# Kernel optimization log

Hardware: AMD Instinct MI355X
Metric: run time of the kernel (lower is better)

## Reference

```python
import jax, jax.numpy as jnp
import numpy as np

# GE2E batch structure: N_SPK speakers, M_UTT utterances each (grouped contiguously),
# first half enrollment (-> centroid), second half test.
N_SPK, M_UTT, D = 1024, 32, 512
M_ENR = M_UTT // 2
EPS = 1e-8  # F.cosine_similarity default eps (clamps norms)


def setup_inputs() -> dict:
    key = jax.random.key(0)
    emb = jax.random.normal(key, (N_SPK * M_UTT, D), dtype=jnp.float32)
    labels = jnp.repeat(jnp.arange(N_SPK, dtype=jnp.int64), M_UTT)
    alpha = jnp.asarray(10.0, dtype=jnp.float32)
    beta = jnp.asarray(-5.0, dtype=jnp.float32)
    return {"embeddings": emb, "labels": labels, "alpha": alpha, "beta": beta}


def reference(embeddings, labels, alpha, beta):
    # labels are contiguously grouped: label i occupies rows [i*M_UTT, (i+1)*M_UTT)
    emb = embeddings.reshape(N_SPK, M_UTT, D)
    enroll = emb[:, :M_ENR]          # [N, M_enr, D]
    test = emb[:, M_ENR:]            # [N, M_tst, D]
    centroid = enroll.mean(axis=1)   # [N, D]

    cent_n = centroid / jnp.maximum(
        jnp.linalg.norm(centroid, axis=-1, keepdims=True), EPS)
    test_n = test / jnp.maximum(
        jnp.linalg.norm(test, axis=-1, keepdims=True), EPS)

    # S[i, j, t] = alpha * cos(centroid_i, test_{j,t}) + beta
    S = alpha * jnp.einsum('id,jtd->ijt', cent_n, test_n) + beta
    E = jnp.exp(S)                                   # [N, N, M_tst]

    idx = jnp.arange(N_SPK)
    pos_sum = E[idx, idx].sum(axis=-1)               # diag: own test vs own centroid
    neg_sum = E.sum(axis=(1, 2)) - pos_sum           # all other speakers' test utts

    loss = (jnp.log(neg_sum) - jnp.log(pos_sum)).mean()
    return loss
```

## Files before the change

### kernel.cpp

```cpp
#include <hip/hip_runtime.h>
#include <math.h>

#define N_SPK 1024
#define M_UTT 32
#define M_ENR 16
#define M_TEST 16
#define D 512
#define N_TEST_ROWS (N_SPK * M_TEST)


typedef __attribute__((ext_vector_type(4))) float f32x4;
typedef __attribute__((ext_vector_type(8))) short short8;
typedef __attribute__((ext_vector_type(8))) unsigned short ushort8;

typedef const __attribute__((address_space(1))) void g_void;
typedef __attribute__((address_space(3))) void lds_void;

__device__ __forceinline__ unsigned short f2bf(float f) {
    unsigned int u = __float_as_uint(f);
    u += 0x7FFF + ((u >> 16) & 1);
    return (unsigned short)(u >> 16);
}

__global__ __launch_bounds__(256) void prep_kernel(const float* __restrict__ emb,
                                                   unsigned short* __restrict__ cent,
                                                   unsigned short* __restrict__ test,
                                                   float* __restrict__ g_row,
                                                   float* __restrict__ g_pos) {
    const int b = blockIdx.x;
    const int tid = threadIdx.x;
    const int lane = tid & 63;
    const int wid = tid >> 6;

    if (b < 4) {
        g_row[b * 256 + tid] = 0.f;
        g_pos[b * 256 + tid] = 0.f;
    }

    if (b < N_SPK) {
        const float* base = emb + (size_t)b * M_UTT * D;
        float a0 = 0.f, a1 = 0.f;
#pragma unroll
        for (int u = 0; u < M_ENR; ++u) {
            a0 += base[u * D + tid];
            a1 += base[u * D + tid + 256];
        }
        a0 *= (1.f / 16.f);
        a1 *= (1.f / 16.f);
        float ss = a0 * a0 + a1 * a1;
#pragma unroll
        for (int m = 1; m < 64; m <<= 1) ss += __shfl_xor(ss, m, 64);
        __shared__ float wss[4];
        if (lane == 0) wss[wid] = ss;
        __syncthreads();
        const float tot = wss[0] + wss[1] + wss[2] + wss[3];
        const float inv = 1.f / fmaxf(sqrtf(tot), 1e-8f);
        cent[b * D + tid] = f2bf(a0 * inv);
        cent[b * D + tid + 256] = f2bf(a1 * inv);
    } else {
        const int r = (b - N_SPK) * 4 + wid;
        const int s = r >> 4, t = r & 15;
        const float* row = emb + ((size_t)s * M_UTT + M_ENR + t) * D;
        const f32x4* rv = (const f32x4*)row;
        const f32x4 v0 = rv[lane * 2];
        const f32x4 v1 = rv[lane * 2 + 1];
        float ss = v0[0]*v0[0] + v0[1]*v0[1] + v0[2]*v0[2] + v0[3]*v0[3]
                 + v1[0]*v1[0] + v1[1]*v1[1] + v1[2]*v1[2] + v1[3]*v1[3];
#pragma unroll
        for (int m = 1; m < 64; m <<= 1) ss += __shfl_xor(ss, m, 64);
        const float inv = 1.f / fmaxf(sqrtf(ss), 1e-8f);
        ushort8 o;
        o[0] = f2bf(v0[0] * inv); o[1] = f2bf(v0[1] * inv);
        o[2] = f2bf(v0[2] * inv); o[3] = f2bf(v0[3] * inv);
        o[4] = f2bf(v1[0] * inv); o[5] = f2bf(v1[1] * inv);
        o[6] = f2bf(v1[2] * inv); o[7] = f2bf(v1[3] * inv);
        *(ushort8*)&test[(size_t)r * D + lane * 8] = o;
    }
}

__global__ __launch_bounds__(512, 2) void gemm_kernel(const unsigned short* __restrict__ A,
                                                      const unsigned short* __restrict__ B,
                                                      const float* __restrict__ alpha_p,
                                                      const float* __restrict__ beta_p,
                                                      float* __restrict__ g_row,
                                                      float* __restrict__ g_pos) {
    __shared__ __align__(16) unsigned short As[128 * 512];
    __shared__ float rowsum[128];
    __shared__ float possum[128];

    const int tid = threadIdx.x;
    const int lane = tid & 63;
    const int w = tid >> 6;

    const int raw = blockIdx.x;
    const int wg = (raw & 7) * 32 + (raw >> 3);
    const int bi = wg & 7;
    const int bj = wg >> 3;
    const int row0 = bi * 128, col0 = bj * 512;
    const bool has_diag = ((bj >> 2) == bi);

#pragma unroll
    for (int it = 0; it < 16; ++it) {
        const int r = it * 8 + w;
        const int src = (row0 + r) * D + ((lane * 8) ^ ((r & 7) << 3));
        __builtin_amdgcn_global_load_lds((g_void*)&A[src],
                                         (lds_void*)&As[r * D],
                                         16, 0, 0);
    }
    if (tid < 128) { rowsum[tid] = 0.f; possum[tid] = 0.f; }

    const float alpha = *alpha_p;
    const float beta = *beta_p;

    const int bcol = col0 + w * 64;
    const unsigned short* bp[4];
#pragma unroll
    for (int ni = 0; ni < 4; ++ni)
        bp[ni] = &B[(size_t)(bcol + ni * 16 + (lane & 15)) * D + (lane >> 4) * 8];

    const int hs = ((lane >> 4) * 8) ^ ((lane & 7) << 3);
    const int arow_base = (lane & 15) * D;

    f32x4 acc[8][4] = {};
    short8 bf0[4], bf1[4];

#define LOADB(dst, kk)                                             \
    {                                                              \
        const int kp_ = (kk);                                      \
        _Pragma("unroll") for (int ni = 0; ni < 4; ++ni)           \
            dst[ni] = *(const short8*)(bp[ni] + kp_);              \
    }

#define STEP(bfr, kk)                                                          \
    {                                                                          \
        const int ofs_ = (kk) ^ hs;                                            \
        _Pragma("unroll") for (int mi = 0; mi < 8; ++mi) {                     \
            const short8 af_ = *(const short8*)&As[mi * 16 * D + arow_base + ofs_]; \
            _Pragma("unroll") for (int ni = 0; ni < 4; ++ni)                   \
                acc[mi][ni] = __builtin_amdgcn_mfma_f32_16x16x32_bf16(         \
                    af_, bfr[ni], acc[mi][ni], 0, 0, 0);                       \
        }                                                                      \
    }

    LOADB(bf0, 0);
    __syncthreads();

    for (int ko = 0; ko < D; ko += 64) {
        LOADB(bf1, ko + 32);
        STEP(bf0, ko);
        LOADB(bf0, (ko + 64) & (D - 1));
        STEP(bf1, ko + 32);
    }

#pragma unroll
    for (int mi = 0; mi < 8; ++mi) {
#pragma unroll
        for (int r = 0; r < 4; ++r) {
            const int lrow = mi * 16 + ((lane >> 4) << 2) + r;
            const int grow = row0 + lrow;
            float tot = 0.f, pos = 0.f;
#pragma unroll
            for (int ni = 0; ni < 4; ++ni) {
                const int gcol = bcol + ni * 16 + (lane & 15);
                const float e = __expf(fmaf(alpha, acc[mi][ni][r], beta));
                tot += e;
                if (has_diag) pos += ((gcol >> 4) == grow) ? e : 0.f;
            }
#pragma unroll
            for (int m = 1; m < 16; m <<= 1) tot += __shfl_xor(tot, m, 64);
            if (has_diag) {
#pragma unroll
                for (int m = 1; m < 16; m <<= 1) pos += __shfl_xor(pos, m, 64);
            }
            if ((lane & 15) == 0) {
                atomicAdd(&rowsum[lrow], tot);
                if (has_diag) atomicAdd(&possum[lrow], pos);
            }
        }
    }
    __syncthreads();
    if (tid < 128) {
        atomicAdd(&g_row[row0 + tid], rowsum[tid]);
        if (has_diag) atomicAdd(&g_pos[row0 + tid], possum[tid]);
    }
#undef LOADB
#undef STEP
}

__global__ __launch_bounds__(1024) void finalize_kernel(const float* __restrict__ g_row,
                                                        const float* __restrict__ g_pos,
                                                        float* __restrict__ out) {
    __shared__ float red[1024];
    const int i = threadIdx.x;
    const float pos = g_pos[i];
    const float neg = g_row[i] - pos;
    red[i] = logf(fmaxf(neg, 1e-30f)) - logf(fmaxf(pos, 1e-30f));
    __syncthreads();
    for (int s = 512; s > 0; s >>= 1) {
        if (i < s) red[i] += red[i + s];
        __syncthreads();
    }
    if (i == 0) out[0] = red[0] * (1.f / 1024.f);
}

extern "C" void kernel_launch(void* const* d_in, const int* in_sizes, int n_in,
                              void* d_out, int out_size, void* d_ws, size_t ws_size,
                              hipStream_t stream) {
    const float* emb = (const float*)d_in[0];
    const float* alpha_p = (const float*)d_in[2];
    const float* beta_p = (const float*)d_in[3];

    unsigned short* cent = (unsigned short*)d_ws;
    unsigned short* test = cent + (size_t)N_SPK * D;
    float* g_row = (float*)(test + (size_t)N_TEST_ROWS * D);
    float* g_pos = g_row + N_SPK;

    prep_kernel<<<N_SPK + N_TEST_ROWS / 4, 256, 0, stream>>>(emb, cent, test, g_row, g_pos);

    gemm_kernel<<<256, 512, 0, stream>>>(cent, test, alpha_p, beta_p, g_row, g_pos);

    finalize_kernel<<<1, 1024, 0, stream>>>(g_row, g_pos, (float*)d_out);
}
```

Measured before the change: 49.09 us.

## Switch similarity GEMM to FP8 scaled MFMA and fuse finalize via last-block reduction

Normalized centroids and test rows are now quantized to FP8 E4M3 instead of BF16, and the GEMM uses the 32x32x64 scaled f8f6f4 MFMA with test rows as the M operand and centroids staged in LDS. The tile mapping changes to 512 blocks, and the separate finalize kernel is removed: a global counter lets the last finishing block compute the log-loss. The aim is to halve operand bandwidth, double matrix throughput and save a kernel launch, at the cost of FP8 precision error inside exp(alpha*cos), which could shift the loss.

```diff
diff --git a/kernel.cpp b/kernel.cpp
--- a/kernel.cpp
+++ b/kernel.cpp
@@ -7,26 +7,43 @@
 #define M_TEST 16
 #define D 512
 #define N_TEST_ROWS (N_SPK * M_TEST)
+#define NBLK_GEMM 512
 
 
 typedef __attribute__((ext_vector_type(4))) float f32x4;
-typedef __attribute__((ext_vector_type(8))) short short8;
-typedef __attribute__((ext_vector_type(8))) unsigned short ushort8;
+typedef __attribute__((ext_vector_type(4))) int i32x4;
+typedef __attribute__((ext_vector_type(8))) int i32x8;
+typedef __attribute__((ext_vector_type(16))) float f32x16;
 
 typedef const __attribute__((address_space(1))) void g_void;
 typedef __attribute__((address_space(3))) void lds_void;
 
-__device__ __forceinline__ unsigned short f2bf(float f) {
+__device__ __forceinline__ unsigned int f2e4m3(float f) {
     unsigned int u = __float_as_uint(f);
-    u += 0x7FFF + ((u >> 16) & 1);
-    return (unsigned short)(u >> 16);
+    const unsigned int s = (u >> 31) << 7;
+    float a = fabsf(f);
+    if (a >= 448.f) return s | 0x7E;
+    unsigned int ua = u & 0x7FFFFFFFu;
+    int e = (int)(ua >> 23) - 127;
+    if (e >= -6) {
+        ua += 0x7FFFF + ((ua >> 20) & 1);
+        e = (int)(ua >> 23) - 127;
+        if (e > 8) return s | 0x7E;
+        const unsigned int m = (ua >> 20) & 7;
+        return s | ((unsigned int)(e + 7) << 3) | m;
+    } else {
+        const int k = (int)rintf(a * 512.f);
+        if (k >= 8) return s | 0x08;
+        return s | (unsigned int)k;
+    }
 }
 
 __global__ __launch_bounds__(256) void prep_kernel(const float* __restrict__ emb,
-                                                   unsigned short* __restrict__ cent,
-                                                   unsigned short* __restrict__ test,
+                                                   unsigned char* __restrict__ cent8,
+                                                   unsigned char* __restrict__ test8,
                                                    float* __restrict__ g_row,
-                                                   float* __restrict__ g_pos) {
+                                                   float* __restrict__ g_pos,
+                                                   unsigned int* __restrict__ cnt) {
     const int b = blockIdx.x;
     const int tid = threadIdx.x;
     const int lane = tid & 63;
@@ -35,6 +52,7 @@
     if (b < 4) {
         g_row[b * 256 + tid] = 0.f;
         g_pos[b * 256 + tid] = 0.f;
+        if (b == 0 && tid == 0) *cnt = 0u;
     }
 
     if (b < N_SPK) {
@@ -55,8 +73,8 @@
         __syncthreads();
         const float tot = wss[0] + wss[1] + wss[2] + wss[3];
         const float inv = 1.f / fmaxf(sqrtf(tot), 1e-8f);
-        cent[b * D + tid] = f2bf(a0 * inv);
-        cent[b * D + tid + 256] = f2bf(a1 * inv);
+        cent8[b * D + tid] = (unsigned char)f2e4m3(a0 * inv);
+        cent8[b * D + tid + 256] = (unsigned char)f2e4m3(a1 * inv);
     } else {
         const int r = (b - N_SPK) * 4 + wid;
         const int s = r >> 4, t = r & 15;
@@ -69,138 +87,166 @@
 #pragma unroll
         for (int m = 1; m < 64; m <<= 1) ss += __shfl_xor(ss, m, 64);
         const float inv = 1.f / fmaxf(sqrtf(ss), 1e-8f);
-        ushort8 o;
-        o[0] = f2bf(v0[0] * inv); o[1] = f2bf(v0[1] * inv);
-        o[2] = f2bf(v0[2] * inv); o[3] = f2bf(v0[3] * inv);
-        o[4] = f2bf(v1[0] * inv); o[5] = f2bf(v1[1] * inv);
-        o[6] = f2bf(v1[2] * inv); o[7] = f2bf(v1[3] * inv);
-        *(ushort8*)&test[(size_t)r * D + lane * 8] = o;
-    }
-}
-
-__global__ __launch_bounds__(512, 2) void gemm_kernel(const unsigned short* __restrict__ A,
-                                                      const unsigned short* __restrict__ B,
-                                                      const float* __restrict__ alpha_p,
-                                                      const float* __restrict__ beta_p,
-                                                      float* __restrict__ g_row,
-                                                      float* __restrict__ g_pos) {
-    __shared__ __align__(16) unsigned short As[128 * 512];
-    __shared__ float rowsum[128];
-    __shared__ float possum[128];
+        unsigned long long ob = 0ull;
+        ob |= (unsigned long long)f2e4m3(v0[0] * inv);
+        ob |= (unsigned long long)f2e4m3(v0[1] * inv) << 8;
+        ob |= (unsigned long long)f2e4m3(v0[2] * inv) << 16;
+        ob |= (unsigned long long)f2e4m3(v0[3] * inv) << 24;
+        ob |= (unsigned long long)f2e4m3(v1[0] * inv) << 32;
+        ob |= (unsigned long long)f2e4m3(v1[1] * inv) << 40;
+        ob |= (unsigned long long)f2e4m3(v1[2] * inv) << 48;
+        ob |= (unsigned long long)f2e4m3(v1[3] * inv) << 56;
+        *(unsigned long long*)&test8[(size_t)r * D + lane * 8] = ob;
+    }
+}
+
+__global__ __launch_bounds__(512) void gemm_kernel(const unsigned char* __restrict__ A,
+                                                   const unsigned char* __restrict__ Bc,
+                                                   const float* __restrict__ alpha_p,
+                                                   const float* __restrict__ beta_p,
+                                                   float* __restrict__ g_row,
+                                                   float* __restrict__ g_pos,
+                                                   unsigned int* __restrict__ cnt,
+                                                   float* __restrict__ out) {
+    __shared__ __align__(16) unsigned char Bs[128 * 512];
+    __shared__ float tsum[128];
+    __shared__ float psum[128];
+    __shared__ unsigned int last_flag;
+    __shared__ float ws2[8];
 
     const int tid = threadIdx.x;
     const int lane = tid & 63;
     const int w = tid >> 6;
-
-    const int raw = blockIdx.x;
-    const int wg = (raw & 7) * 32 + (raw >> 3);
-    const int bi = wg & 7;
-    const int bj = wg >> 3;
-    const int row0 = bi * 128, col0 = bj * 512;
-    const bool has_diag = ((bj >> 2) == bi);
-
-#pragma unroll
-    for (int it = 0; it < 16; ++it) {
-        const int r = it * 8 + w;
-        const int src = (row0 + r) * D + ((lane * 8) ^ ((r & 7) << 3));
-        __builtin_amdgcn_global_load_lds((g_void*)&A[src],
-                                         (lds_void*)&As[r * D],
-                                         16, 0, 0);
-    }
-    if (tid < 128) { rowsum[tid] = 0.f; possum[tid] = 0.f; }
+    const int wr = w >> 1;
+    const int wc = w & 1;
+    const int hh = lane >> 5;
+    const int l31 = lane & 31;
+
+    const int bid = blockIdx.x;
+    const int idx = bid >> 3;
+    const int bm = (bid & 7) * 8 + (idx & 7);
+    const int bn = idx >> 3;
+    const bool has_diag = (bn == (bm >> 3));
+
+#pragma unroll
+    for (int it = 0; it < 8; ++it) {
+        const int q = it * 8 + w;
+        const int r_l = 2 * q + hh;
+        const int src_col = (l31 ^ (r_l & 31)) << 4;
+        __builtin_amdgcn_global_load_lds(
+            (g_void*)&Bc[(size_t)(bn * 128 + r_l) * D + src_col],
+            (lds_void*)&Bs[(2 * q) * 512],
+            16, 0, 0);
+    }
+    if (tid < 128) { tsum[tid] = 0.f; psum[tid] = 0.f; }
 
     const float alpha = *alpha_p;
     const float beta = *beta_p;
 
-    const int bcol = col0 + w * 64;
-    const unsigned short* bp[4];
-#pragma unroll
-    for (int ni = 0; ni < 4; ++ni)
-        bp[ni] = &B[(size_t)(bcol + ni * 16 + (lane & 15)) * D + (lane >> 4) * 8];
-
-    const int hs = ((lane >> 4) * 8) ^ ((lane & 7) << 3);
-    const int arow_base = (lane & 15) * D;
-
-    f32x4 acc[8][4] = {};
-    short8 bf0[4], bf1[4];
-
-#define LOADB(dst, kk)                                             \
-    {                                                              \
-        const int kp_ = (kk);                                      \
-        _Pragma("unroll") for (int ni = 0; ni < 4; ++ni)           \
-            dst[ni] = *(const short8*)(bp[ni] + kp_);              \
-    }
-
-#define STEP(bfr, kk)                                                          \
-    {                                                                          \
-        const int ofs_ = (kk) ^ hs;                                            \
-        _Pragma("unroll") for (int mi = 0; mi < 8; ++mi) {                     \
-            const short8 af_ = *(const short8*)&As[mi * 16 * D + arow_base + ofs_]; \
-            _Pragma("unroll") for (int ni = 0; ni < 4; ++ni)                   \
-                acc[mi][ni] = __builtin_amdgcn_mfma_f32_16x16x32_bf16(         \
-                    af_, bfr[ni], acc[mi][ni], 0, 0, 0);                       \
-        }                                                                      \
-    }
-
-    LOADB(bf0, 0);
+    const int mrow0 = bm * 256 + wr * 64;
+    const int ncol0 = bn * 128 + wc * 64;
+
+    const unsigned char* pa0 = A + (size_t)(mrow0 + l31) * D + hh * 32;
+    const unsigned char* pa1 = A + (size_t)(mrow0 + 32 + l31) * D + hh * 32;
+    const int rb0 = (wc * 64 + l31) * 512;
+    const int rb1 = rb0 + 32 * 512;
+
+    f32x16 acc00 = (f32x16)(0.0f), acc01 = (f32x16)(0.0f);
+    f32x16 acc10 = (f32x16)(0.0f), acc11 = (f32x16)(0.0f);
+    i32x8 A00, A01, A10, A11, B00, B01, B10, B11;
+
+#define ALOAD(d0, d1, s)                                                        \
+    { i32x4 lo = *(const i32x4*)(pa0 + (s) * 64);                               \
+      i32x4 hi = *(const i32x4*)(pa0 + (s) * 64 + 16);                          \
+      d0 = __builtin_shufflevector(lo, hi, 0, 1, 2, 3, 4, 5, 6, 7);             \
+      lo = *(const i32x4*)(pa1 + (s) * 64);                                     \
+      hi = *(const i32x4*)(pa1 + (s) * 64 + 16);                                \
+      d1 = __builtin_shufflevector(lo, hi, 0, 1, 2, 3, 4, 5, 6, 7); }
+
+#define BLOAD(d0, d1, s)                                                        \
+    { const int G0 = (s) * 4 + hh * 2;                                          \
+      i32x4 lo = *(const i32x4*)&Bs[rb0 + ((G0 ^ l31) << 4)];                   \
+      i32x4 hi = *(const i32x4*)&Bs[rb0 + (((G0 + 1) ^ l31) << 4)];             \
+      d0 = __builtin_shufflevector(lo, hi, 0, 1, 2, 3, 4, 5, 6, 7);             \
+      lo = *(const i32x4*)&Bs[rb1 + ((G0 ^ l31) << 4)];                         \
+      hi = *(const i32x4*)&Bs[rb1 + (((G0 + 1) ^ l31) << 4)];                   \
+      d1 = __builtin_shufflevector(lo, hi, 0, 1, 2, 3, 4, 5, 6, 7); }
+
+#define MSTEP(Aa0, Aa1, Bb0, Bb1)                                               \
+    acc00 = __builtin_amdgcn_mfma_scale_f32_32x32x64_f8f6f4(                    \
+        Aa0, Bb0, acc00, 0, 0, 0, 0x7F7F7F7F, 0, 0x7F7F7F7F);                   \
+    acc01 = __builtin_amdgcn_mfma_scale_f32_32x32x64_f8f6f4(                    \
+        Aa0, Bb1, acc01, 0, 0, 0, 0x7F7F7F7F, 0, 0x7F7F7F7F);                   \
+    acc10 = __builtin_amdgcn_mfma_scale_f32_32x32x64_f8f6f4(                    \
+        Aa1, Bb0, acc10, 0, 0, 0, 0x7F7F7F7F, 0, 0x7F7F7F7F);                   \
+    acc11 = __builtin_amdgcn_mfma_scale_f32_32x32x64_f8f6f4(                    \
+        Aa1, Bb1, acc11, 0, 0, 0, 0x7F7F7F7F, 0, 0x7F7F7F7F);
+
+    ALOAD(A00, A01, 0);
     __syncthreads();
-
-    for (int ko = 0; ko < D; ko += 64) {
-        LOADB(bf1, ko + 32);
-        STEP(bf0, ko);
-        LOADB(bf0, (ko + 64) & (D - 1));
-        STEP(bf1, ko + 32);
-    }
-
-#pragma unroll
-    for (int mi = 0; mi < 8; ++mi) {
-#pragma unroll
-        for (int r = 0; r < 4; ++r) {
-            const int lrow = mi * 16 + ((lane >> 4) << 2) + r;
-            const int grow = row0 + lrow;
-            float tot = 0.f, pos = 0.f;
-#pragma unroll
-            for (int ni = 0; ni < 4; ++ni) {
-                const int gcol = bcol + ni * 16 + (lane & 15);
-                const float e = __expf(fmaf(alpha, acc[mi][ni][r], beta));
-                tot += e;
-                if (has_diag) pos += ((gcol >> 4) == grow) ? e : 0.f;
-            }
-#pragma unroll
-            for (int m = 1; m < 16; m <<= 1) tot += __shfl_xor(tot, m, 64);
-            if (has_diag) {
-#pragma unroll
-                for (int m = 1; m < 16; m <<= 1) pos += __shfl_xor(pos, m, 64);
-            }
-            if ((lane & 15) == 0) {
-                atomicAdd(&rowsum[lrow], tot);
-                if (has_diag) atomicAdd(&possum[lrow], pos);
-            }
-        }
-    }
+    BLOAD(B00, B01, 0); ALOAD(A10, A11, 1); BLOAD(B10, B11, 1);
+
+    MSTEP(A00, A01, B00, B01); ALOAD(A00, A01, 2); BLOAD(B00, B01, 2);
+    MSTEP(A10, A11, B10, B11); ALOAD(A10, A11, 3); BLOAD(B10, B11, 3);
+    MSTEP(A00, A01, B00, B01); ALOAD(A00, A01, 4); BLOAD(B00, B01, 4);
+    MSTEP(A10, A11, B10, B11); ALOAD(A10, A11, 5); BLOAD(B10, B11, 5);
+    MSTEP(A00, A01, B00, B01); ALOAD(A00, A01, 6); BLOAD(B00, B01, 6);
+    MSTEP(A10, A11, B10, B11); ALOAD(A10, A11, 7); BLOAD(B10, B11, 7);
+    MSTEP(A00, A01, B00, B01);
+    MSTEP(A10, A11, B10, B11);
+#undef ALOAD
+#undef BLOAD
+#undef MSTEP
+
+#define EPI(ACC, mi, ni)                                                        \
+    {                                                                           \
+        float t = 0.f, p = 0.f;                                                 \
+        _Pragma("unroll") for (int r = 0; r < 16; ++r) {                        \
+            const float e = __expf(fmaf(alpha, ACC[r], beta));                  \
+            t += e;                                                             \
+            if (has_diag) {                                                     \
+                const int row = mrow0 + (mi) * 32 + (r & 3) + 8 * (r >> 2) + 4 * hh; \
+                p += (((row >> 4) == (ncol0 + (ni) * 32 + l31)) ? e : 0.f);     \
+            }                                                                   \
+        }                                                                       \
+        t += __shfl_xor(t, 32, 64);                                             \
+        if (lane < 32) atomicAdd(&tsum[wc * 64 + (ni) * 32 + l31], t);          \
+        if (has_diag) {                                                         \
+            p += __shfl_xor(p, 32, 64);                                         \
+            if (lane < 32) atomicAdd(&psum[wc * 64 + (ni) * 32 + l31], p);      \
+        }                                                                       \
+    }
+    EPI(acc00, 0, 0) EPI(acc01, 0, 1) EPI(acc10, 1, 0) EPI(acc11, 1, 1)
+#undef EPI
+
     __syncthreads();
     if (tid < 128) {
-        atomicAdd(&g_row[row0 + tid], rowsum[tid]);
-        if (has_diag) atomicAdd(&g_pos[row0 + tid], possum[tid]);
-    }
-#undef LOADB
-#undef STEP
-}
-
-__global__ __launch_bounds__(1024) void finalize_kernel(const float* __restrict__ g_row,
-                                                        const float* __restrict__ g_pos,
-                                                        float* __restrict__ out) {
-    __shared__ float red[1024];
-    const int i = threadIdx.x;
-    const float pos = g_pos[i];
-    const float neg = g_row[i] - pos;
-    red[i] = logf(fmaxf(neg, 1e-30f)) - logf(fmaxf(pos, 1e-30f));
+        atomicAdd(&g_row[bn * 128 + tid], tsum[tid]);
+        if (has_diag) atomicAdd(&g_pos[bn * 128 + tid], psum[tid]);
+    }
+
+    __threadfence();
+    if (tid == 0) last_flag = (atomicAdd(cnt, 1u) == (NBLK_GEMM - 1)) ? 1u : 0u;
     __syncthreads();
-    for (int s = 512; s > 0; s >>= 1) {
-        if (i < s) red[i] += red[i + s];
+    if (last_flag) {
+        __threadfence();
+        float v = 0.f;
+        for (int i = tid; i < N_SPK; i += 512) {
+            const float pos = g_pos[i];
+            const float neg = g_row[i] - pos;
+            v += logf(fmaxf(neg, 1e-30f)) - logf(fmaxf(pos, 1e-30f));
+        }
+#pragma unroll
+        for (int m = 1; m < 64; m <<= 1) v += __shfl_xor(v, m, 64);
+        if (lane == 0) ws2[w] = v;
         __syncthreads();
-    }
-    if (i == 0) out[0] = red[0] * (1.f / 1024.f);
+        if (tid == 0) {
+            float s = 0.f;
+#pragma unroll
+            for (int j = 0; j < 8; ++j) s += ws2[j];
+            out[0] = s * (1.f / 1024.f);
+        }
+    }
 }
 
 extern "C" void kernel_launch(void* const* d_in, const int* in_sizes, int n_in,
@@ -210,14 +256,15 @@
     const float* alpha_p = (const float*)d_in[2];
     const float* beta_p = (const float*)d_in[3];
 
-    unsigned short* cent = (unsigned short*)d_ws;
-    unsigned short* test = cent + (size_t)N_SPK * D;
-    float* g_row = (float*)(test + (size_t)N_TEST_ROWS * D);
+    unsigned char* cent8 = (unsigned char*)d_ws;
+    unsigned char* test8 = cent8 + (size_t)N_SPK * D;
+    float* g_row = (float*)(test8 + (size_t)N_TEST_ROWS * D);
     float* g_pos = g_row + N_SPK;
-
-    prep_kernel<<<N_SPK + N_TEST_ROWS / 4, 256, 0, stream>>>(emb, cent, test, g_row, g_pos);
-
-    gemm_kernel<<<256, 512, 0, stream>>>(cent, test, alpha_p, beta_p, g_row, g_pos);
-
-    finalize_kernel<<<1, 1024, 0, stream>>>(g_row, g_pos, (float*)d_out);
-}
+    unsigned int* cnt = (unsigned int*)(g_pos + N_SPK);
+
+    prep_kernel<<<N_SPK + N_TEST_ROWS / 4, 256, 0, stream>>>(emb, cent8, test8,
+                                                             g_row, g_pos, cnt);
+
+    gemm_kernel<<<NBLK_GEMM, 512, 0, stream>>>(test8, cent8, alpha_p, beta_p,
+                                               g_row, g_pos, cnt, (float*)d_out);
+}
```

After: 98.70 us. 101% more time.
